# Kernel tuning notes

Measured on AMD Instinct MI355X. Metric: run time of the kernel, lower is better.

## Reference

```python
import jax, jax.numpy as jnp
import numpy as np

H_DIM = 64
GRID = 8
NS = 2.0  # neighborhood_size


def _pool_seq(hidden, pos):
    # hidden: (P, H_DIM) hidden states of peds in one scene; pos: (P, 2) end positions
    P = hidden.shape[0]
    g2 = GRID * GRID
    tl_x = pos[:, 0] - NS / 2
    tl_y = pos[:, 1] + NS / 2
    br_x = pos[:, 0] + NS / 2
    br_y = pos[:, 1] - NS / 2
    # pair (i, j): grid of ped i (rows), position of ped j (cols)
    ox = pos[None, :, 0]
    oy = pos[None, :, 1]
    cell_x = jnp.floor((ox - tl_x[:, None]) / NS * GRID)
    cell_y = jnp.floor((tl_y[:, None] - oy) / NS * GRID)
    grid_pos = (cell_x + cell_y * GRID).astype(jnp.int32)
    # out-of-bound if outside neighborhood box OR i == j (diagonal forced out)
    oob = ((ox >= br_x[:, None]) | (ox <= tl_x[:, None])
           | (oy >= tl_y[:, None]) | (oy <= br_y[:, None])
           | jnp.eye(P, dtype=bool))
    idx = grid_pos + 1 + (jnp.arange(P, dtype=jnp.int32) * g2)[:, None]
    idx = jnp.where(oob, 0, idx)  # slot 0 is the trash bin (dropped below)
    src = jnp.broadcast_to(hidden[None], (P, P, H_DIM)).reshape(P * P, H_DIM)
    buf = jnp.zeros((P * g2 + 1, H_DIM), hidden.dtype)
    buf = buf.at[idx.reshape(-1)].add(src)
    return buf[1:].reshape(P, g2 * H_DIM)


def reference(h_states, seq_start_end, end_pos, rel_pos, W, b):
    B = end_pos.shape[0]
    S = seq_start_end.shape[0]
    P = B // S  # equal-length scenes -> static reshape
    hidden = h_states.reshape(-1, H_DIM).reshape(S, P, H_DIM)
    pos = end_pos.reshape(S, P, 2)
    pooled = jax.vmap(_pool_seq)(hidden, pos).reshape(B, GRID * GRID * H_DIM)
    # make_mlp([4096, 1024], relu, batch_norm=False): Linear -> ReLU
    return jax.nn.relu(pooled @ W + b)


def setup_inputs():
    key = jax.random.key(0)
    k0, k1, k2, k3 = jax.random.split(key, 4)
    S, P = 64, 64
    B = S * P
    bottleneck = 1024
    feat = GRID * GRID * H_DIM  # 4096
    h_states = jax.random.normal(k0, (1, B, H_DIM), jnp.float32)
    starts = jnp.arange(S, dtype=jnp.int32) * P
    seq_start_end = jnp.stack([starts, starts + P], axis=1)
    end_pos = jax.random.normal(k1, (B, 2), jnp.float32)
    rel_pos = jax.random.normal(k2, (B, 2), jnp.float32)
    W = jax.random.normal(k3, (feat, bottleneck), jnp.float32) * 0.02
    b = jnp.zeros((bottleneck,), jnp.float32)
    return {"h_states": h_states, "seq_start_end": seq_start_end,
            "end_pos": end_pos, "rel_pos": rel_pos, "W": W, "b": b}
```

## Files before the change

### kernel.cpp

```cpp
#include <hip/hip_runtime.h>


#define BM 128
#define BN 64
#define BK 128

typedef short short8 __attribute__((ext_vector_type(8)));
typedef short short4v __attribute__((ext_vector_type(4)));
typedef float floatx4 __attribute__((ext_vector_type(4)));

__device__ inline short f2bf(float x) {
    union { float f; unsigned u; } v; v.f = x;
    unsigned r = v.u + 0x7fffu + ((v.u >> 16) & 1u);
    return (short)(r >> 16);
}

__device__ inline void gload_lds16(const void* g, void* l) {
    __builtin_amdgcn_global_load_lds(
        (const __attribute__((address_space(1))) void*)g,
        (__attribute__((address_space(3))) void*)l,
        16, 0, 0);
}

__global__ __launch_bounds__(256) void pool_kernel(
    const float* __restrict__ h,
    const float* __restrict__ pos,
    short* __restrict__ pooled)
{
    __shared__ float hs[64 * 64];
    __shared__ float px[64], py[64];
    __shared__ unsigned long long wmask[4][64];

    const int tid  = threadIdx.x;
    const int lane = tid & 63;
    const int w    = tid >> 6;
    const int s    = blockIdx.x >> 4;
    const int grp  = blockIdx.x & 15;
    const size_t base = (size_t)s * 64;

    const float4* hv  = (const float4*)(h + base * 64);
    float4*       hsv = (float4*)hs;
    #pragma unroll
    for (int c = 0; c < 4; ++c) hsv[tid + c * 256] = hv[tid + c * 256];
    if (tid < 64) {
        float2 p = ((const float2*)pos)[base + tid];
        px[tid] = p.x; py[tid] = p.y;
    }
    wmask[w][lane] = 0ull;
    __syncthreads();

    const int i = grp * 4 + w;
    const float tlx = px[i] - 1.0f;
    const float tly = py[i] + 1.0f;
    const float brx = px[i] + 1.0f;
    const float bry = py[i] - 1.0f;

    {
        const int j = lane;
        const float ox = px[j], oy = py[j];
        if (ox < brx && ox > tlx && oy < tly && oy > bry && j != i) {
            int cx = (int)floorf((ox - tlx) * 4.0f);
            int cy = (int)floorf((tly - oy) * 4.0f);
            atomicOr(&wmask[w][cx + cy * 8], 1ull << j);
        }
    }

    const int d = lane;
    const size_t orow = (base + i) * 4096;
    for (int c = 0; c < 64; ++c) {
        unsigned long long m = wmask[w][c];
        float a0 = 0.f, a1 = 0.f;
        while (m) {
            int j0 = __builtin_ctzll(m); m &= m - 1;
            if (m) {
                int j1 = __builtin_ctzll(m); m &= m - 1;
                a1 += hs[j1 * 64 + d];
            }
            a0 += hs[j0 * 64 + d];
        }
        pooled[orow + c * 64 + d] = f2bf(a0 + a1);
    }
}

__global__ __launch_bounds__(256) void castWt_kernel(
    const float* __restrict__ W, short* __restrict__ Wt, int K, int N)
{
    __shared__ float t[64][65];
    const int tid = threadIdx.x;
    const int k0 = blockIdx.x * 64;
    const int n0 = blockIdx.y * 64;

    const int r  = tid >> 4;
    const int cq = (tid & 15) * 4;
    #pragma unroll
    for (int i = 0; i < 4; ++i) {
        const int row = r + i * 16;
        float4 v = *(const float4*)&W[(size_t)(k0 + row) * N + n0 + cq];
        t[row][cq + 0] = v.x; t[row][cq + 1] = v.y;
        t[row][cq + 2] = v.z; t[row][cq + 3] = v.w;
    }
    __syncthreads();
    const int nl = tid >> 4;
    const int kq = (tid & 15) * 4;
    #pragma unroll
    for (int i = 0; i < 4; ++i) {
        const int n = nl + i * 16;
        short4v o;
        o.x = f2bf(t[kq + 0][n]); o.y = f2bf(t[kq + 1][n]);
        o.z = f2bf(t[kq + 2][n]); o.w = f2bf(t[kq + 3][n]);
        *(short4v*)&Wt[(size_t)(n0 + n) * K + k0 + kq] = o;
    }
}

__global__ __launch_bounds__(256) void gemm_bias_relu(
    const short* __restrict__ A,
    const short* __restrict__ Bt,
    const float* __restrict__ bias,
    float* __restrict__ out,
    int M, int N, int K)
{
    __shared__ __align__(16) short As[BM * BK];
    __shared__ __align__(16) short Bs[BN * BK];

    const int tid  = threadIdx.x;
    const int lane = tid & 63;
    const int wave = tid >> 6;
    const int wr = wave >> 1;
    const int wc = wave & 1;
    const int q  = lane >> 4;
    const int ml = lane & 15;
    const int m0 = blockIdx.y * BM;
    const int n0 = blockIdx.x * BN;

    const int r4   = lane >> 4;
    const int slot = lane & 15;

    const short* ag[8];
    const short* bg[4];
    #pragma unroll
    for (int c = 0; c < 8; ++c) {
        const int gi = c * 4 + wave;
        const int rl = gi * 4 + r4;
        ag[c] = A + (size_t)(m0 + rl) * K + (slot ^ (rl & 15)) * 8;
    }
    #pragma unroll
    for (int c = 0; c < 4; ++c) {
        const int gi = c * 4 + wave;
        const int rl = gi * 4 + r4;
        bg[c] = Bt + (size_t)(n0 + rl) * K + (slot ^ (rl & 15)) * 8;
    }

    floatx4 acc[4][2];
    #pragma unroll
    for (int i = 0; i < 4; ++i)
        #pragma unroll
        for (int j = 0; j < 2; ++j)
            acc[i][j] = (floatx4){0.f, 0.f, 0.f, 0.f};

    for (int kb = 0; kb < K; kb += BK) {
        if (kb) __syncthreads();
        #pragma unroll
        for (int c = 0; c < 8; ++c) {
            gload_lds16(ag[c], &As[(c * 4 + wave) * 512]);
            ag[c] += BK;
        }
        #pragma unroll
        for (int c = 0; c < 4; ++c) {
            gload_lds16(bg[c], &Bs[(c * 4 + wave) * 512]);
            bg[c] += BK;
        }
        __syncthreads();

        #pragma unroll
        for (int t = 0; t < 4; ++t) {
            short8 af[4], bf[2];
            const int gx = ((t * 4 + q) ^ ml) * 8;
            #pragma unroll
            for (int i = 0; i < 4; ++i)
                af[i] = *(const short8*)&As[(wr * 64 + i * 16 + ml) * BK + gx];
            #pragma unroll
            for (int j = 0; j < 2; ++j)
                bf[j] = *(const short8*)&Bs[(wc * 32 + j * 16 + ml) * BK + gx];
            #pragma unroll
            for (int i = 0; i < 4; ++i)
                #pragma unroll
                for (int j = 0; j < 2; ++j)
                    acc[i][j] = __builtin_amdgcn_mfma_f32_16x16x32_bf16(
                        af[i], bf[j], acc[i][j], 0, 0, 0);
        }
    }

    #pragma unroll
    for (int j = 0; j < 2; ++j) {
        const int gn = n0 + wc * 32 + j * 16 + ml;
        const float bv = bias[gn];
        #pragma unroll
        for (int i = 0; i < 4; ++i) {
            const int gm = m0 + wr * 64 + i * 16 + q * 4;
            #pragma unroll
            for (int r = 0; r < 4; ++r) {
                float v = acc[i][j][r] + bv;
                out[(size_t)(gm + r) * N + gn] = v > 0.f ? v : 0.f;
            }
        }
    }
}

extern "C" void kernel_launch(void* const* d_in, const int* in_sizes, int n_in,
                              void* d_out, int out_size, void* d_ws, size_t ws_size,
                              hipStream_t stream) {
    const float* h    = (const float*)d_in[0];
    const float* pos  = (const float*)d_in[2];
    const float* W    = (const float*)d_in[4];
    const float* bias = (const float*)d_in[5];

    const int B = in_sizes[0] / 64;
    const int S = in_sizes[1] / 2;
    const int N = in_sizes[5];
    const int K = 64 * 64;
    (void)S;

    short* pooled = (short*)d_ws;
    short* Wt     = pooled + (size_t)B * K;
    float* out    = (float*)d_out;

    pool_kernel<<<B / 4, 256, 0, stream>>>(h, pos, pooled);
    castWt_kernel<<<dim3(K / 64, N / 64), 256, 0, stream>>>(W, Wt, K, N);
    gemm_bias_relu<<<dim3(N / BN, B / BM), 256, 0, stream>>>(pooled, Wt, bias, out, B, N, K);
}
```

Baseline: 141.3 us.

## Merge pool and weight-cast kernels; double-buffer GEMM with split-K waves

Merges the pooling and weight transpose-cast kernels into one launch, with each block choosing its role from its block index. This removes a launch and lets the two independent jobs overlap. The GEMM now uses a 128x128 tile with BK=64 and 512 threads. Two groups of four waves each take half of every K step, and their partial sums are combined through LDS at the end. Global-to-LDS loads are double-buffered so the next tile is fetched during the MFMAs, at the cost of more LDS per block, a reduction step, and fewer blocks in the grid.

```diff
diff --git a/kernel.cpp b/kernel.cpp
--- a/kernel.cpp
+++ b/kernel.cpp
@@ -2,8 +2,8 @@
 
 
 #define BM 128
-#define BN 64
-#define BK 128
+#define BN 128
+#define BK 64
 
 typedef short short8 __attribute__((ext_vector_type(8)));
 typedef short short4v __attribute__((ext_vector_type(4)));
@@ -22,186 +22,209 @@
         16, 0, 0);
 }
 
-__global__ __launch_bounds__(256) void pool_kernel(
+__global__ __launch_bounds__(256) void prep_kernel(
     const float* __restrict__ h,
     const float* __restrict__ pos,
-    short* __restrict__ pooled)
+    short* __restrict__ pooled,
+    const float* __restrict__ W,
+    short* __restrict__ Wt,
+    int K, int N, int poolBlocks)
 {
-    __shared__ float hs[64 * 64];
-    __shared__ float px[64], py[64];
-    __shared__ unsigned long long wmask[4][64];
-
-    const int tid  = threadIdx.x;
-    const int lane = tid & 63;
-    const int w    = tid >> 6;
-    const int s    = blockIdx.x >> 4;
-    const int grp  = blockIdx.x & 15;
-    const size_t base = (size_t)s * 64;
-
-    const float4* hv  = (const float4*)(h + base * 64);
-    float4*       hsv = (float4*)hs;
-    #pragma unroll
-    for (int c = 0; c < 4; ++c) hsv[tid + c * 256] = hv[tid + c * 256];
-    if (tid < 64) {
-        float2 p = ((const float2*)pos)[base + tid];
-        px[tid] = p.x; py[tid] = p.y;
-    }
-    wmask[w][lane] = 0ull;
-    __syncthreads();
-
-    const int i = grp * 4 + w;
-    const float tlx = px[i] - 1.0f;
-    const float tly = py[i] + 1.0f;
-    const float brx = px[i] + 1.0f;
-    const float bry = py[i] - 1.0f;
-
-    {
-        const int j = lane;
-        const float ox = px[j], oy = py[j];
-        if (ox < brx && ox > tlx && oy < tly && oy > bry && j != i) {
-            int cx = (int)floorf((ox - tlx) * 4.0f);
-            int cy = (int)floorf((tly - oy) * 4.0f);
-            atomicOr(&wmask[w][cx + cy * 8], 1ull << j);
-        }
-    }
-
-    const int d = lane;
-    const size_t orow = (base + i) * 4096;
-    for (int c = 0; c < 64; ++c) {
-        unsigned long long m = wmask[w][c];
-        float a0 = 0.f, a1 = 0.f;
-        while (m) {
-            int j0 = __builtin_ctzll(m); m &= m - 1;
-            if (m) {
-                int j1 = __builtin_ctzll(m); m &= m - 1;
-                a1 += hs[j1 * 64 + d];
+    __shared__ __align__(16) unsigned char sh[18944];
+    const int tid = threadIdx.x;
+
+    if ((int)blockIdx.x < poolBlocks) {
+        float* hs = (float*)sh;
+        float* px = (float*)(sh + 16384);
+        float* py = (float*)(sh + 16640);
+        unsigned long long* wmask = (unsigned long long*)(sh + 16896);
+
+        const int lane = tid & 63;
+        const int w    = tid >> 6;
+        const int s    = blockIdx.x >> 4;
+        const int grp  = blockIdx.x & 15;
+        const size_t base = (size_t)s * 64;
+
+        const float4* hv  = (const float4*)(h + base * 64);
+        float4*       hsv = (float4*)hs;
+        #pragma unroll
+        for (int c = 0; c < 4; ++c) hsv[tid + c * 256] = hv[tid + c * 256];
+        if (tid < 64) {
+            float2 p = ((const float2*)pos)[base + tid];
+            px[tid] = p.x; py[tid] = p.y;
+        }
+        wmask[w * 64 + lane] = 0ull;
+        __syncthreads();
+
+        const int i = grp * 4 + w;
+        const float tlx = px[i] - 1.0f;
+        const float tly = py[i] + 1.0f;
+        const float brx = px[i] + 1.0f;
+        const float bry = py[i] - 1.0f;
+
+        {
+            const int j = lane;
+            const float ox = px[j], oy = py[j];
+            if (ox < brx && ox > tlx && oy < tly && oy > bry && j != i) {
+                int cx = (int)floorf((ox - tlx) * 4.0f);
+                int cy = (int)floorf((tly - oy) * 4.0f);
+                atomicOr(&wmask[w * 64 + cx + cy * 8], 1ull << j);
             }
-            a0 += hs[j0 * 64 + d];
-        }
-        pooled[orow + c * 64 + d] = f2bf(a0 + a1);
-    }
-}
-
-__global__ __launch_bounds__(256) void castWt_kernel(
-    const float* __restrict__ W, short* __restrict__ Wt, int K, int N)
-{
-    __shared__ float t[64][65];
-    const int tid = threadIdx.x;
-    const int k0 = blockIdx.x * 64;
-    const int n0 = blockIdx.y * 64;
-
-    const int r  = tid >> 4;
-    const int cq = (tid & 15) * 4;
-    #pragma unroll
-    for (int i = 0; i < 4; ++i) {
-        const int row = r + i * 16;
-        float4 v = *(const float4*)&W[(size_t)(k0 + row) * N + n0 + cq];
-        t[row][cq + 0] = v.x; t[row][cq + 1] = v.y;
-        t[row][cq + 2] = v.z; t[row][cq + 3] = v.w;
-    }
-    __syncthreads();
-    const int nl = tid >> 4;
-    const int kq = (tid & 15) * 4;
-    #pragma unroll
-    for (int i = 0; i < 4; ++i) {
-        const int n = nl + i * 16;
-        short4v o;
-        o.x = f2bf(t[kq + 0][n]); o.y = f2bf(t[kq + 1][n]);
-        o.z = f2bf(t[kq + 2][n]); o.w = f2bf(t[kq + 3][n]);
-        *(short4v*)&Wt[(size_t)(n0 + n) * K + k0 + kq] = o;
-    }
-}
-
-__global__ __launch_bounds__(256) void gemm_bias_relu(
+        }
+        __builtin_amdgcn_s_waitcnt(0);
+
+        const int d = lane;
+        const size_t orow = (base + i) * 4096;
+        for (int c = 0; c < 64; ++c) {
+            unsigned long long m = wmask[w * 64 + c];
+            float a0 = 0.f, a1 = 0.f;
+            while (m) {
+                int j0 = __builtin_ctzll(m); m &= m - 1;
+                if (m) {
+                    int j1 = __builtin_ctzll(m); m &= m - 1;
+                    a1 += hs[j1 * 64 + d];
+                }
+                a0 += hs[j0 * 64 + d];
+            }
+            pooled[orow + c * 64 + d] = f2bf(a0 + a1);
+        }
+    } else {
+        float* t = (float*)sh;
+        const int bid = blockIdx.x - poolBlocks;
+        const int k0 = (bid & 63) * 64;
+        const int n0 = (bid >> 6) * 64;
+
+        const int r  = tid >> 4;
+        const int cq = (tid & 15) * 4;
+        #pragma unroll
+        for (int i2 = 0; i2 < 4; ++i2) {
+            const int row = r + i2 * 16;
+            float4 v = *(const float4*)&W[(size_t)(k0 + row) * N + n0 + cq];
+            t[row * 65 + cq + 0] = v.x; t[row * 65 + cq + 1] = v.y;
+            t[row * 65 + cq + 2] = v.z; t[row * 65 + cq + 3] = v.w;
+        }
+        __syncthreads();
+        const int nl = tid >> 4;
+        const int kq = (tid & 15) * 4;
+        #pragma unroll
+        for (int i2 = 0; i2 < 4; ++i2) {
+            const int n = nl + i2 * 16;
+            short4v o;
+            o.x = f2bf(t[(kq + 0) * 65 + n]); o.y = f2bf(t[(kq + 1) * 65 + n]);
+            o.z = f2bf(t[(kq + 2) * 65 + n]); o.w = f2bf(t[(kq + 3) * 65 + n]);
+            *(short4v*)&Wt[(size_t)(n0 + n) * K + k0 + kq] = o;
+        }
+    }
+}
+
+__global__ __launch_bounds__(512, 2) void gemm_bias_relu(
     const short* __restrict__ A,
     const short* __restrict__ Bt,
     const float* __restrict__ bias,
     float* __restrict__ out,
     int M, int N, int K)
 {
-    __shared__ __align__(16) short As[BM * BK];
-    __shared__ __align__(16) short Bs[BN * BK];
+    __shared__ __align__(16) short smem[2][2][BM * BK];
 
     const int tid  = threadIdx.x;
     const int lane = tid & 63;
     const int wave = tid >> 6;
-    const int wr = wave >> 1;
-    const int wc = wave & 1;
+    const int kg = wave >> 2;
+    const int w4 = wave & 3;
+    const int wr = w4 >> 1;
+    const int wc = w4 & 1;
     const int q  = lane >> 4;
     const int ml = lane & 15;
     const int m0 = blockIdx.y * BM;
     const int n0 = blockIdx.x * BN;
 
-    const int r4   = lane >> 4;
-    const int slot = lane & 15;
-
-    const short* ag[8];
-    const short* bg[4];
+    const int r8    = lane >> 3;
+    const int slot3 = lane & 7;
+
+    const short* ag[2];
+    const short* bg[2];
+    int agrp[2];
     #pragma unroll
-    for (int c = 0; c < 8; ++c) {
-        const int gi = c * 4 + wave;
-        const int rl = gi * 4 + r4;
-        ag[c] = A + (size_t)(m0 + rl) * K + (slot ^ (rl & 15)) * 8;
-    }
-    #pragma unroll
-    for (int c = 0; c < 4; ++c) {
-        const int gi = c * 4 + wave;
-        const int rl = gi * 4 + r4;
-        bg[c] = Bt + (size_t)(n0 + rl) * K + (slot ^ (rl & 15)) * 8;
-    }
-
-    floatx4 acc[4][2];
+    for (int c = 0; c < 2; ++c) {
+        const int g  = c * 8 + wave;
+        const int rl = g * 8 + r8;
+        agrp[c] = g;
+        ag[c] = A  + (size_t)(m0 + rl) * K + (slot3 ^ (rl & 7)) * 8;
+        bg[c] = Bt + (size_t)(n0 + rl) * K + (slot3 ^ (rl & 7)) * 8;
+    }
+
+    floatx4 acc[4][4];
     #pragma unroll
     for (int i = 0; i < 4; ++i)
         #pragma unroll
-        for (int j = 0; j < 2; ++j)
+        for (int j = 0; j < 4; ++j)
             acc[i][j] = (floatx4){0.f, 0.f, 0.f, 0.f};
 
+    #pragma unroll
+    for (int c = 0; c < 2; ++c) {
+        gload_lds16(ag[c], &smem[0][0][agrp[c] * 512]);
+        gload_lds16(bg[c], &smem[0][1][agrp[c] * 512]);
+        ag[c] += BK; bg[c] += BK;
+    }
+    __syncthreads();
+
+    int buf = 0;
+    const int gxg = ((kg * 4 + q) ^ (ml & 7)) * 8;
     for (int kb = 0; kb < K; kb += BK) {
-        if (kb) __syncthreads();
-        #pragma unroll
-        for (int c = 0; c < 8; ++c) {
-            gload_lds16(ag[c], &As[(c * 4 + wave) * 512]);
-            ag[c] += BK;
-        }
-        #pragma unroll
-        for (int c = 0; c < 4; ++c) {
-            gload_lds16(bg[c], &Bs[(c * 4 + wave) * 512]);
-            bg[c] += BK;
-        }
+        if (kb + BK < K) {
+            #pragma unroll
+            for (int c = 0; c < 2; ++c) {
+                gload_lds16(ag[c], &smem[buf ^ 1][0][agrp[c] * 512]);
+                gload_lds16(bg[c], &smem[buf ^ 1][1][agrp[c] * 512]);
+                ag[c] += BK; bg[c] += BK;
+            }
+        }
+        short8 af[4], bf[4];
+        #pragma unroll
+        for (int i = 0; i < 4; ++i)
+            af[i] = *(const short8*)&smem[buf][0][(wr * 64 + i * 16 + ml) * BK + gxg];
+        #pragma unroll
+        for (int j = 0; j < 4; ++j)
+            bf[j] = *(const short8*)&smem[buf][1][(wc * 64 + j * 16 + ml) * BK + gxg];
+        #pragma unroll
+        for (int i = 0; i < 4; ++i)
+            #pragma unroll
+            for (int j = 0; j < 4; ++j)
+                acc[i][j] = __builtin_amdgcn_mfma_f32_16x16x32_bf16(
+                    af[i], bf[j], acc[i][j], 0, 0, 0);
+
         __syncthreads();
-
-        #pragma unroll
-        for (int t = 0; t < 4; ++t) {
-            short8 af[4], bf[2];
-            const int gx = ((t * 4 + q) ^ ml) * 8;
-            #pragma unroll
-            for (int i = 0; i < 4; ++i)
-                af[i] = *(const short8*)&As[(wr * 64 + i * 16 + ml) * BK + gx];
-            #pragma unroll
-            for (int j = 0; j < 2; ++j)
-                bf[j] = *(const short8*)&Bs[(wc * 32 + j * 16 + ml) * BK + gx];
+        buf ^= 1;
+    }
+
+    float* xp = (float*)smem + w4 * 4096;
+    if (kg == 1) {
+        #pragma unroll
+        for (int i = 0; i < 4; ++i)
+            #pragma unroll
+            for (int j = 0; j < 4; ++j)
+                #pragma unroll
+                for (int r = 0; r < 4; ++r) {
+                    const int row = i * 16 + q * 4 + r;
+                    const int col = (j * 16 + ml + q * 8) & 63;
+                    xp[row * 64 + col] = acc[i][j][r];
+                }
+    }
+    __syncthreads();
+    if (kg == 0) {
+        #pragma unroll
+        for (int j = 0; j < 4; ++j) {
+            const int gn = n0 + wc * 64 + j * 16 + ml;
+            const float bv = bias[gn];
             #pragma unroll
             for (int i = 0; i < 4; ++i)
                 #pragma unroll
-                for (int j = 0; j < 2; ++j)
-                    acc[i][j] = __builtin_amdgcn_mfma_f32_16x16x32_bf16(
-                        af[i], bf[j], acc[i][j], 0, 0, 0);
-        }
-    }
-
-    #pragma unroll
-    for (int j = 0; j < 2; ++j) {
-        const int gn = n0 + wc * 32 + j * 16 + ml;
-        const float bv = bias[gn];
-        #pragma unroll
-        for (int i = 0; i < 4; ++i) {
-            const int gm = m0 + wr * 64 + i * 16 + q * 4;
-            #pragma unroll
-            for (int r = 0; r < 4; ++r) {
-                float v = acc[i][j][r] + bv;
-                out[(size_t)(gm + r) * N + gn] = v > 0.f ? v : 0.f;
-            }
+                for (int r = 0; r < 4; ++r) {
+                    const int row = i * 16 + q * 4 + r;
+                    const int col = (j * 16 + ml + q * 8) & 63;
+                    float v = acc[i][j][r] + xp[row * 64 + col] + bv;
+                    out[(size_t)(m0 + wr * 64 + row) * N + gn] = v > 0.f ? v : 0.f;
+                }
         }
     }
 }
@@ -215,16 +238,17 @@
     const float* bias = (const float*)d_in[5];
 
     const int B = in_sizes[0] / 64;
-    const int S = in_sizes[1] / 2;
     const int N = in_sizes[5];
     const int K = 64 * 64;
-    (void)S;
 
     short* pooled = (short*)d_ws;
     short* Wt     = pooled + (size_t)B * K;
     float* out    = (float*)d_out;
 
-    pool_kernel<<<B / 4, 256, 0, stream>>>(h, pos, pooled);
-    castWt_kernel<<<dim3(K / 64, N / 64), 256, 0, stream>>>(W, Wt, K, N);
-    gemm_bias_relu<<<dim3(N / BN, B / BM), 256, 0, stream>>>(pooled, Wt, bias, out, B, N, K);
-}
+    const int poolBlocks = B / 4;
+    const int castBlocks = (K / 64) * (N / 64);
+    prep_kernel<<<poolBlocks + castBlocks, 256, 0, stream>>>(
+        h, pos, pooled, W, Wt, K, N, poolBlocks);
+    gemm_bias_relu<<<dim3(N / BN, B / BM), 512, 0, stream>>>(
+        pooled, Wt, bias, out, B, N, K);
+}
```

Measured after the change: 141.0 us. Within noise of the previous version (-0.2%).
